# Kernel tuning notes

Hardware: AMD Instinct MI355X
Metric: run time of the kernel (lower is better)

## Reference

```python
import jax, jax.numpy as jnp
import numpy as np


def setup_inputs() -> dict:
    key = jax.random.key(0)
    k1, k2, k3, k4 = jax.random.split(key, 4)
    B, T, D, U = 32, 2048, 256, 256
    x = jax.random.normal(k1, (B, T, D), dtype=jnp.float32)
    Wz = jax.random.normal(k2, (D + U, U), dtype=jnp.float32) * 0.05
    Wr = jax.random.normal(k3, (D + U, U), dtype=jnp.float32) * 0.05
    Wh = jax.random.normal(k4, (D + U, U), dtype=jnp.float32) * 0.05
    return {"x": x, "Wz": Wz, "Wr": Wr, "Wh": Wh}


def reference(x, Wz, Wr, Wh):
    # GRU recurrence: z = sigmoid([x,h] Wz); r = sigmoid([x,h] Wr);
    # h_hat = tanh([x, r*h] Wh); h' = z*h + (1-z)*h_hat
    B = x.shape[0]
    U = Wz.shape[1]
    h0 = jnp.zeros((B, U), dtype=x.dtype)

    def step(h, x_t):
        x_h = jnp.concatenate([x_t, h], axis=-1)          # [B, D+U]
        z = jax.nn.sigmoid(x_h @ Wz)                       # [B, U]
        r = jax.nn.sigmoid(x_h @ Wr)                       # [B, U]
        x_rh = jnp.concatenate([x_t, r * h], axis=-1)      # [B, D+U]
        h_hat = jnp.tanh(x_rh @ Wh)                        # [B, U]
        new_h = z * h + (1.0 - z) * h_hat
        return new_h, new_h

    xs = jnp.swapaxes(x, 0, 1)                             # [T, B, D]
    _, ys = jax.lax.scan(step, h0, xs)                     # ys: [T, B, U]
    return jnp.swapaxes(ys, 0, 1)                          # [B, T, U]
```

## Files before the change

kernel.cpp:

```cpp
#include <hip/hip_runtime.h>
#include <hip/hip_fp16.h>
#include <stdint.h>

#define NB 32
#define NT 2048
#define ND 256
#define NU 256

typedef _Float16 f16x2 __attribute__((ext_vector_type(2)));

__device__ __forceinline__ float fdot2u(uint32_t a, uint32_t b, float c) {
#if __has_builtin(__builtin_amdgcn_fdot2)
  return __builtin_amdgcn_fdot2(__builtin_bit_cast(f16x2, a),
                                __builtin_bit_cast(f16x2, b), c, false);
#else
  f16x2 av = __builtin_bit_cast(f16x2, a);
  f16x2 bv = __builtin_bit_cast(f16x2, b);
  return c + (float)av.x * (float)bv.x + (float)av.y * (float)bv.y;
#endif
}

__device__ __forceinline__ uint32_t packh2(float lo, float hi) {
  f16x2 p;
  p.x = (_Float16)lo;
  p.y = (_Float16)hi;
  return __builtin_bit_cast(uint32_t, p);
}

__device__ __forceinline__ uint4 ldg_opaque(const uint4* p) {
  uint4 r;
  asm volatile("global_load_dwordx4 %0, %1, off" : "=v"(r) : "v"(p));
  return r;
}

__device__ __forceinline__ float rcp_fast(float x) { return __builtin_amdgcn_rcpf(x); }
__device__ __forceinline__ float sigmoid_fast(float x) {
  return rcp_fast(1.f + __expf(-x));
}
__device__ __forceinline__ float tanh_fast(float x) {
  return 1.f - 2.f * rcp_fast(1.f + __expf(2.f * x));
}

struct SRec {
  float hbuf[NU];
  alignas(16) uint32_t h2[NU / 2];
  alignas(16) uint32_t rh2[NU / 2];
  float psh[NU];
};
struct SGemm {
  float a[64][132];
  float b[64][68];
};

__global__ __launch_bounds__(512, 2)
__attribute__((amdgpu_waves_per_eu(2, 2)))
void gru_combined(
    const float* __restrict__ x, const float* __restrict__ Wz,
    const float* __restrict__ Wr, const float* __restrict__ Wh,
    const uint32_t* __restrict__ Wf16, float* __restrict__ hstate,
    float* __restrict__ out, const float* __restrict__ Gsrc,
    float* __restrict__ Gdst, int t0r, int t0g, int recCnt, int chunkT) {
  __shared__ union SM {
    SRec r;
    SGemm g;
  } sm;
  const int tid = threadIdx.x;

  if ((int)blockIdx.x < recCnt) {
    const int b = blockIdx.x;
    const int u = tid & (NU - 1);
    const int role = tid >> 8;

    uint4 wfull[32], wh[16];
    const uint4* W4 = (const uint4*)Wf16;
    const uint4* pf = W4 + (size_t)role * (NU * 32) + u * 32;
#pragma unroll
    for (int j = 0; j < 32; j++) wfull[j] = ldg_opaque(pf + j);
    const uint4* ph = W4 + (size_t)2 * (NU * 32) + u * 32 + role * 16;
#pragma unroll
    for (int j = 0; j < 16; j++) wh[j] = ldg_opaque(ph + j);

    float hu = hstate[b * NU + u];
    if (tid < NU) sm.r.hbuf[tid] = hu;
    __syncthreads();
    if (tid < NU / 2) sm.r.h2[tid] = packh2(sm.r.hbuf[2 * tid], sm.r.hbuf[2 * tid + 1]);
    __syncthreads();

    asm volatile("s_waitcnt vmcnt(0)" ::: "memory");
    __builtin_amdgcn_sched_barrier(0);

    const float* Gb = Gsrc + (size_t)b * NU + u;
    float* outp = out + ((size_t)b * NT + t0r) * NU + u;
    float hprev = hu;

    for (int tt = 0; tt < chunkT; ++tt) {
      float g0, g1 = 0.f;
      {
        const float* Gt = Gb + (size_t)(tt * 3) * NB * NU;
        if (role == 0) {
          g0 = Gt[0];
          g1 = Gt[2 * NB * NU];
        } else {
          g0 = Gt[NB * NU];
        }
      }
      float a0 = 0.f, a1 = 0.f, a2 = 0.f, a3 = 0.f;
#pragma unroll
      for (int jb = 0; jb < 32; jb++) {
        uint4 hv = *(const uint4*)&sm.r.h2[jb * 4];
        a0 = fdot2u(wfull[jb].x, hv.x, a0);
        a1 = fdot2u(wfull[jb].y, hv.y, a1);
        a2 = fdot2u(wfull[jb].z, hv.z, a2);
        a3 = fdot2u(wfull[jb].w, hv.w, a3);
      }
      const float ssum = ((a0 + a1) + (a2 + a3)) + g0;
      float zval = 0.f;
      if (role == 1) {
        const float rr = sigmoid_fast(ssum);
        const float rh = rr * hprev;
        const float rh1 = __shfl_down(rh, 1);
        if ((u & 1) == 0) sm.r.rh2[u >> 1] = packh2(rh, rh1);
      } else {
        zval = sigmoid_fast(ssum);
      }
      __syncthreads();
      float c0 = 0.f, c1 = 0.f, c2 = 0.f, c3 = 0.f;
#pragma unroll
      for (int jb = 0; jb < 16; jb++) {
        uint4 rv = *(const uint4*)&sm.r.rh2[(role * 16 + jb) * 4];
        c0 = fdot2u(wh[jb].x, rv.x, c0);
        c1 = fdot2u(wh[jb].y, rv.y, c1);
        c2 = fdot2u(wh[jb].z, rv.z, c2);
        c3 = fdot2u(wh[jb].w, rv.w, c3);
      }
      const float csum = (c0 + c1) + (c2 + c3);
      if (role == 1) sm.r.psh[u] = csum;
      __syncthreads();
      if (role == 0) {
        const float hh = tanh_fast(g1 + csum + sm.r.psh[u]);
        const float hn = zval * hprev + (1.f - zval) * hh;
        hprev = hn;
        outp[0] = hn;
        sm.r.hbuf[u] = hn;
        const float hn1 = __shfl_down(hn, 1);
        if ((u & 1) == 0) sm.r.h2[u >> 1] = packh2(hn, hn1);
      }
      outp += NU;
      __syncthreads();
      if (role == 1) hprev = sm.r.hbuf[u];
    }
    if (role == 0) hstate[b * NU + u] = hprev;

  } else if (Gdst != nullptr) {
    const int gg = (int)blockIdx.x - recCnt;
    const int mtile = gg / 12;
    const int ntile = gg - mtile * 12;
    const int g = ntile >> 2;
    const int u0 = (ntile & 3) * 64;
    const float* Wg = (g == 0) ? Wz : ((g == 1) ? Wr : Wh);
    const int ty = tid >> 4;
    const int tx = tid & 15;
    const int mbase = mtile * 128;
    float acc[4][4] = {{0.f}};

    for (int kk = 0; kk < 4; ++kk) {
      const int k0 = kk * 64;
      __syncthreads();
      {
        const int ml = tid & 127;
        const int kq = tid >> 7;
        const int m = mbase + ml;
        const int bb = m / chunkT;
        const int tt = m - bb * chunkT;
        const float* xp = x + ((size_t)bb * NT + t0g + tt) * ND + k0 + kq * 16;
#pragma unroll
        for (int v = 0; v < 4; ++v) {
          float4 xv = ((const float4*)xp)[v];
          sm.g.a[kq * 16 + v * 4 + 0][ml] = xv.x;
          sm.g.a[kq * 16 + v * 4 + 1][ml] = xv.y;
          sm.g.a[kq * 16 + v * 4 + 2][ml] = xv.z;
          sm.g.a[kq * 16 + v * 4 + 3][ml] = xv.w;
        }
      }
      {
        const int nl = (tid & 15) * 4;
        const int kr = tid >> 4;
#pragma unroll
        for (int s = 0; s < 2; ++s) {
          const int krow = kr + s * 32;
          float4 wv = *(const float4*)&Wg[(size_t)(k0 + krow) * NU + u0 + nl];
          *(float4*)&sm.g.b[krow][nl] = wv;
        }
      }
      __syncthreads();
#pragma unroll 8
      for (int k = 0; k < 64; ++k) {
        const float4 av = *(const float4*)&sm.g.a[k][ty * 4];
        const float4 bv = *(const float4*)&sm.g.b[k][tx * 4];
        acc[0][0] += av.x * bv.x; acc[0][1] += av.x * bv.y; acc[0][2] += av.x * bv.z; acc[0][3] += av.x * bv.w;
        acc[1][0] += av.y * bv.x; acc[1][1] += av.y * bv.y; acc[1][2] += av.y * bv.z; acc[1][3] += av.y * bv.w;
        acc[2][0] += av.z * bv.x; acc[2][1] += av.z * bv.y; acc[2][2] += av.z * bv.z; acc[2][3] += av.z * bv.w;
        acc[3][0] += av.w * bv.x; acc[3][1] += av.w * bv.y; acc[3][2] += av.w * bv.z; acc[3][3] += av.w * bv.w;
      }
    }
#pragma unroll
    for (int i = 0; i < 4; ++i) {
      const int m = mbase + ty * 4 + i;
      const int bb = m / chunkT;
      const int tt = m - bb * chunkT;
      float4 val;
      val.x = acc[i][0]; val.y = acc[i][1]; val.z = acc[i][2]; val.w = acc[i][3];
      *(float4*)&Gdst[((size_t)(tt * 3 + g) * NB + bb) * NU + u0 + tx * 4] = val;
    }
  }
}

__global__ void gru_prep(const float* __restrict__ Wz, const float* __restrict__ Wr,
                         const float* __restrict__ Wh, uint32_t* __restrict__ Wf16,
                         float* __restrict__ hstate) {
  const int idx = blockIdx.x * 256 + threadIdx.x;
  const int NW = 3 * NU * 128;
  if (idx < NW) {
    const int g = idx / (NU * 128);
    const int rem = idx - g * (NU * 128);
    const int u = rem >> 7;
    const int p = rem & 127;
    const float* Wg = (g == 0) ? Wz : ((g == 1) ? Wr : Wh);
    float w0 = Wg[(size_t)(ND + 2 * p) * NU + u];
    float w1 = Wg[(size_t)(ND + 2 * p + 1) * NU + u];
    Wf16[idx] = packh2(w0, w1);
  } else {
    const int j = idx - NW;
    if (j < NB * NU) hstate[j] = 0.f;
  }
}

extern "C" void kernel_launch(void* const* d_in, const int* in_sizes, int n_in,
                              void* d_out, int out_size, void* d_ws, size_t ws_size,
                              hipStream_t stream) {
  (void)in_sizes; (void)n_in; (void)out_size;
  const float* x = (const float*)d_in[0];
  const float* Wz = (const float*)d_in[1];
  const float* Wr = (const float*)d_in[2];
  const float* Wh = (const float*)d_in[3];
  float* out = (float*)d_out;

  int ct = 8;
  const int cands[6] = {256, 128, 64, 32, 16, 8};
  for (int i = 0; i < 6; ++i) {
    size_t need = 2ull * cands[i] * 3 * NB * NU * 4 + (1u << 20);
    if (need <= ws_size) { ct = cands[i]; break; }
  }
  const int nch = NT / ct;
  const size_t chunkBytes = (size_t)ct * 3 * NB * NU * 4;

  char* wsb = (char*)d_ws;
  float* G0 = (float*)wsb;
  float* G1 = (float*)(wsb + chunkBytes);
  uint32_t* Wf16 = (uint32_t*)(wsb + 2 * chunkBytes);
  float* hstate = (float*)(wsb + 2 * chunkBytes + (size_t)3 * NU * 128 * 4);

  const int prepThreads = 3 * NU * 128 + NB * NU;
  gru_prep<<<(prepThreads + 255) / 256, 256, 0, stream>>>(Wz, Wr, Wh, Wf16, hstate);

  gru_combined<<<3 * ct, 512, 0, stream>>>(x, Wz, Wr, Wh, Wf16, hstate, out,
                                           nullptr, G0, 0, 0, 0, ct);
  for (int k = 0; k < nch; ++k) {
    float* Gsrc = (k & 1) ? G1 : G0;
    float* Gdst = (k & 1) ? G0 : G1;
    const int gemmOn = (k + 1 < nch) ? 1 : 0;
    gru_combined<<<32 + (gemmOn ? 3 * ct : 0), 512, 0, stream>>>(
        x, Wz, Wr, Wh, Wf16, hstate, out, Gsrc, gemmOn ? Gdst : nullptr,
        k * ct, (k + 1) * ct, 32, ct);
  }
}
```

Measured before the change: 2.926 ms.

## Move candidate-gate weights to LDS and re-stream z/r weights each step

The fp16 recurrent Wh weights now live in a 128KB dynamic LDS buffer instead of per-thread registers. The z/r weights use a new packed layout and are re-issued as global loads every timestep, after the gate dot products, so they refill while the Wh phase runs. Per-step G loads become inline asm with explicit waitcnts. This frees registers at the cost of heavy per-step L2 traffic. It also forces one large-LDS block per CU, which limits occupancy for the co-scheduled GEMM blocks.

```diff
diff --git a/kernel.cpp b/kernel.cpp
--- a/kernel.cpp
+++ b/kernel.cpp
@@ -27,12 +27,6 @@
   return __builtin_bit_cast(uint32_t, p);
 }
 
-__device__ __forceinline__ uint4 ldg_opaque(const uint4* p) {
-  uint4 r;
-  asm volatile("global_load_dwordx4 %0, %1, off" : "=v"(r) : "v"(p));
-  return r;
-}
-
 __device__ __forceinline__ float rcp_fast(float x) { return __builtin_amdgcn_rcpf(x); }
 __device__ __forceinline__ float sigmoid_fast(float x) {
   return rcp_fast(1.f + __expf(-x));
@@ -41,117 +35,158 @@
   return 1.f - 2.f * rcp_fast(1.f + __expf(2.f * x));
 }
 
-struct SRec {
-  float hbuf[NU];
-  alignas(16) uint32_t h2[NU / 2];
-  alignas(16) uint32_t rh2[NU / 2];
-  float psh[NU];
-};
+#define LDS_WH 0
+#define LDS_H2 131072
+#define LDS_RH2 131584
+#define LDS_PSH 132096
+#define LDS_HBUF 133120
+#define LDS_TOTAL 134144
+
+extern __shared__ char smdyn[];
+
 struct SGemm {
   float a[64][132];
   float b[64][68];
 };
 
-__global__ __launch_bounds__(512, 2)
+#define WDECL \
+  uint4 w0, w1, w2, w3, w4, w5, w6, w7, w8, w9, w10, w11, w12, w13, w14, w15, \
+      w16, w17, w18, w19, w20, w21, w22, w23, w24, w25, w26, w27, w28, w29,   \
+      w30, w31;
+
+#define WL(i, P, OFF) \
+  asm volatile("global_load_dwordx4 %0, %1, off" OFF : "=v"(w##i) : "v"(P));
+
+#define WGRP(i0, i1, i2, i3, P) \
+  WL(i0, P, "") WL(i1, P, " offset:16") WL(i2, P, " offset:32") WL(i3, P, " offset:48")
+
+#define WISSUE \
+  WGRP(0, 1, 2, 3, pA) WGRP(4, 5, 6, 7, pB) WGRP(8, 9, 10, 11, pC) \
+  WGRP(12, 13, 14, 15, pD) WGRP(16, 17, 18, 19, pE) WGRP(20, 21, 22, 23, pF) \
+  WGRP(24, 25, 26, 27, pG) WGRP(28, 29, 30, 31, pH)
+
+#define DOTA(i)                                     \
+  {                                                 \
+    const uint4 hv = *(const uint4*)&h2L[(i) * 4];  \
+    a0 = fdot2u(w##i.x, hv.x, a0);                  \
+    a1 = fdot2u(w##i.y, hv.y, a1);                  \
+    a2 = fdot2u(w##i.z, hv.z, a2);                  \
+    a3 = fdot2u(w##i.w, hv.w, a3);                  \
+  }
+#define DOTA8(i0, i1, i2, i3, i4, i5, i6, i7) \
+  DOTA(i0) DOTA(i1) DOTA(i2) DOTA(i3) DOTA(i4) DOTA(i5) DOTA(i6) DOTA(i7)
+
+__global__ __launch_bounds__(512)
 __attribute__((amdgpu_waves_per_eu(2, 2)))
 void gru_combined(
     const float* __restrict__ x, const float* __restrict__ Wz,
     const float* __restrict__ Wr, const float* __restrict__ Wh,
-    const uint32_t* __restrict__ Wf16, float* __restrict__ hstate,
+    const uint32_t* __restrict__ Wp, float* __restrict__ hstate,
     float* __restrict__ out, const float* __restrict__ Gsrc,
     float* __restrict__ Gdst, int t0r, int t0g, int recCnt, int chunkT) {
-  __shared__ union SM {
-    SRec r;
-    SGemm g;
-  } sm;
   const int tid = threadIdx.x;
 
   if ((int)blockIdx.x < recCnt) {
     const int b = blockIdx.x;
-    const int u = tid & (NU - 1);
+    const int u = tid & 255;
     const int role = tid >> 8;
 
-    uint4 wfull[32], wh[16];
-    const uint4* W4 = (const uint4*)Wf16;
-    const uint4* pf = W4 + (size_t)role * (NU * 32) + u * 32;
-#pragma unroll
-    for (int j = 0; j < 32; j++) wfull[j] = ldg_opaque(pf + j);
-    const uint4* ph = W4 + (size_t)2 * (NU * 32) + u * 32 + role * 16;
-#pragma unroll
-    for (int j = 0; j < 16; j++) wh[j] = ldg_opaque(ph + j);
-
-    float hu = hstate[b * NU + u];
-    if (tid < NU) sm.r.hbuf[tid] = hu;
+    uint32_t* WhL = (uint32_t*)(smdyn + LDS_WH);
+    uint32_t* h2L = (uint32_t*)(smdyn + LDS_H2);
+    uint32_t* rh2L = (uint32_t*)(smdyn + LDS_RH2);
+    float* pshL = (float*)(smdyn + LDS_PSH);
+    float* hbufL = (float*)(smdyn + LDS_HBUF);
+
+    const uint4* colb = ((const uint4*)Wp) + (size_t)role * 8192 + (u << 2);
+    const uint4* pA = colb;
+    const uint4* pB = colb + 1024;
+    const uint4* pC = colb + 2048;
+    const uint4* pD = colb + 3072;
+    const uint4* pE = colb + 4096;
+    const uint4* pF = colb + 5120;
+    const uint4* pG = colb + 6144;
+    const uint4* pH = colb + 7168;
+    WDECL
+    WISSUE
+
+    {
+      const uint4* WpH4 = ((const uint4*)Wp) + 16384;
+      uint4* WhL4 = (uint4*)(smdyn + LDS_WH);
+#pragma unroll
+      for (int i = 0; i < 16; ++i) WhL4[tid + i * 512] = WpH4[tid + i * 512];
+    }
+    float hprev = hstate[b * NU + u];
+    if (tid < NU) hbufL[tid] = hprev;
     __syncthreads();
-    if (tid < NU / 2) sm.r.h2[tid] = packh2(sm.r.hbuf[2 * tid], sm.r.hbuf[2 * tid + 1]);
+    if (tid < 128) h2L[tid] = packh2(hbufL[2 * tid], hbufL[2 * tid + 1]);
     __syncthreads();
 
-    asm volatile("s_waitcnt vmcnt(0)" ::: "memory");
-    __builtin_amdgcn_sched_barrier(0);
-
-    const float* Gb = Gsrc + (size_t)b * NU + u;
+    const char* gp = (const char*)(Gsrc + (size_t)b * NU + u) +
+                     (role == 0 ? 0 : (size_t)NB * NU * 4);
+    const size_t gstride = (size_t)3 * NB * NU * 4;
     float* outp = out + ((size_t)b * NT + t0r) * NU + u;
-    float hprev = hu;
 
     for (int tt = 0; tt < chunkT; ++tt) {
-      float g0, g1 = 0.f;
-      {
-        const float* Gt = Gb + (size_t)(tt * 3) * NB * NU;
-        if (role == 0) {
-          g0 = Gt[0];
-          g1 = Gt[2 * NB * NU];
-        } else {
-          g0 = Gt[NB * NU];
-        }
-      }
+      asm volatile("s_waitcnt vmcnt(0)" ::: "memory");
+      __builtin_amdgcn_sched_barrier(0);
+      float gA, gB = 0.f;
+      asm volatile("global_load_dword %0, %1, off" : "=v"(gA) : "v"(gp));
+      if (role == 0)
+        asm volatile("global_load_dword %0, %1, off"
+                     : "=v"(gB)
+                     : "v"(gp + 2 * (size_t)NB * NU * 4));
       float a0 = 0.f, a1 = 0.f, a2 = 0.f, a3 = 0.f;
-#pragma unroll
-      for (int jb = 0; jb < 32; jb++) {
-        uint4 hv = *(const uint4*)&sm.r.h2[jb * 4];
-        a0 = fdot2u(wfull[jb].x, hv.x, a0);
-        a1 = fdot2u(wfull[jb].y, hv.y, a1);
-        a2 = fdot2u(wfull[jb].z, hv.z, a2);
-        a3 = fdot2u(wfull[jb].w, hv.w, a3);
-      }
-      const float ssum = ((a0 + a1) + (a2 + a3)) + g0;
+      DOTA8(0, 1, 2, 3, 4, 5, 6, 7)
+      DOTA8(8, 9, 10, 11, 12, 13, 14, 15)
+      DOTA8(16, 17, 18, 19, 20, 21, 22, 23)
+      DOTA8(24, 25, 26, 27, 28, 29, 30, 31)
+      asm volatile("s_waitcnt vmcnt(0)" ::: "memory");
+      __builtin_amdgcn_sched_barrier(0);
+      const float ssum = ((a0 + a1) + (a2 + a3)) + gA;
       float zval = 0.f;
-      if (role == 1) {
+      if (role == 0) {
+        zval = sigmoid_fast(ssum);
+      } else {
         const float rr = sigmoid_fast(ssum);
         const float rh = rr * hprev;
         const float rh1 = __shfl_down(rh, 1);
-        if ((u & 1) == 0) sm.r.rh2[u >> 1] = packh2(rh, rh1);
-      } else {
-        zval = sigmoid_fast(ssum);
-      }
+        if ((u & 1) == 0) rh2L[u >> 1] = packh2(rh, rh1);
+      }
+      __builtin_amdgcn_sched_barrier(0);
+      WISSUE
       __syncthreads();
       float c0 = 0.f, c1 = 0.f, c2 = 0.f, c3 = 0.f;
 #pragma unroll
-      for (int jb = 0; jb < 16; jb++) {
-        uint4 rv = *(const uint4*)&sm.r.rh2[(role * 16 + jb) * 4];
-        c0 = fdot2u(wh[jb].x, rv.x, c0);
-        c1 = fdot2u(wh[jb].y, rv.y, c1);
-        c2 = fdot2u(wh[jb].z, rv.z, c2);
-        c3 = fdot2u(wh[jb].w, rv.w, c3);
-      }
-      const float csum = (c0 + c1) + (c2 + c3);
-      if (role == 1) sm.r.psh[u] = csum;
+      for (int j = 0; j < 64; j += 4) {
+        const int k2 = (role << 6) + j;
+        const uint4 r4 = *(const uint4*)&rh2L[k2];
+        c0 = fdot2u(WhL[(k2 + 0) * 256 + u], r4.x, c0);
+        c1 = fdot2u(WhL[(k2 + 1) * 256 + u], r4.y, c1);
+        c2 = fdot2u(WhL[(k2 + 2) * 256 + u], r4.z, c2);
+        c3 = fdot2u(WhL[(k2 + 3) * 256 + u], r4.w, c3);
+      }
+      const float cown = (c0 + c1) + (c2 + c3);
+      if (role == 1) pshL[u] = cown;
       __syncthreads();
       if (role == 0) {
-        const float hh = tanh_fast(g1 + csum + sm.r.psh[u]);
+        const float hh = tanh_fast(gB + cown + pshL[u]);
         const float hn = zval * hprev + (1.f - zval) * hh;
         hprev = hn;
-        outp[0] = hn;
-        sm.r.hbuf[u] = hn;
+        asm volatile("global_store_dword %0, %1, off" ::"v"(outp), "v"(hn));
+        hbufL[u] = hn;
         const float hn1 = __shfl_down(hn, 1);
-        if ((u & 1) == 0) sm.r.h2[u >> 1] = packh2(hn, hn1);
+        if ((u & 1) == 0) h2L[u >> 1] = packh2(hn, hn1);
       }
       outp += NU;
-      __syncthreads();
-      if (role == 1) hprev = sm.r.hbuf[u];
+      gp += gstride;
+      __syncthreads();
+      if (role == 1) hprev = hbufL[u];
     }
     if (role == 0) hstate[b * NU + u] = hprev;
+    asm volatile("s_waitcnt vmcnt(0)" ::: "memory");
 
   } else if (Gdst != nullptr) {
+    SGemm& smg = *(SGemm*)smdyn;
     const int gg = (int)blockIdx.x - recCnt;
     const int mtile = gg / 12;
     const int ntile = gg - mtile * 12;
@@ -171,32 +206,32 @@
         const int kq = tid >> 7;
         const int m = mbase + ml;
         const int bb = m / chunkT;
-        const int tt = m - bb * chunkT;
-        const float* xp = x + ((size_t)bb * NT + t0g + tt) * ND + k0 + kq * 16;
+        const int ttm = m - bb * chunkT;
+        const float* xp = x + ((size_t)bb * NT + t0g + ttm) * ND + k0 + kq * 16;
 #pragma unroll
         for (int v = 0; v < 4; ++v) {
           float4 xv = ((const float4*)xp)[v];
-          sm.g.a[kq * 16 + v * 4 + 0][ml] = xv.x;
-          sm.g.a[kq * 16 + v * 4 + 1][ml] = xv.y;
-          sm.g.a[kq * 16 + v * 4 + 2][ml] = xv.z;
-          sm.g.a[kq * 16 + v * 4 + 3][ml] = xv.w;
+          smg.a[kq * 16 + v * 4 + 0][ml] = xv.x;
+          smg.a[kq * 16 + v * 4 + 1][ml] = xv.y;
+          smg.a[kq * 16 + v * 4 + 2][ml] = xv.z;
+          smg.a[kq * 16 + v * 4 + 3][ml] = xv.w;
         }
       }
       {
         const int nl = (tid & 15) * 4;
         const int kr = tid >> 4;
 #pragma unroll
-        for (int s = 0; s < 2; ++s) {
-          const int krow = kr + s * 32;
-          float4 wv = *(const float4*)&Wg[(size_t)(k0 + krow) * NU + u0 + nl];
-          *(float4*)&sm.g.b[krow][nl] = wv;
+        for (int s2 = 0; s2 < 2; ++s2) {
+          const int krow = kr + s2 * 32;
+          float4 wvv = *(const float4*)&Wg[(size_t)(k0 + krow) * NU + u0 + nl];
+          *(float4*)&smg.b[krow][nl] = wvv;
         }
       }
       __syncthreads();
 #pragma unroll 8
       for (int k = 0; k < 64; ++k) {
-        const float4 av = *(const float4*)&sm.g.a[k][ty * 4];
-        const float4 bv = *(const float4*)&sm.g.b[k][tx * 4];
+        const float4 av = *(const float4*)&smg.a[k][ty * 4];
+        const float4 bv = *(const float4*)&smg.b[k][tx * 4];
         acc[0][0] += av.x * bv.x; acc[0][1] += av.x * bv.y; acc[0][2] += av.x * bv.z; acc[0][3] += av.x * bv.w;
         acc[1][0] += av.y * bv.x; acc[1][1] += av.y * bv.y; acc[1][2] += av.y * bv.z; acc[1][3] += av.y * bv.w;
         acc[2][0] += av.z * bv.x; acc[2][1] += av.z * bv.y; acc[2][2] += av.z * bv.z; acc[2][3] += av.z * bv.w;
@@ -207,31 +242,35 @@
     for (int i = 0; i < 4; ++i) {
       const int m = mbase + ty * 4 + i;
       const int bb = m / chunkT;
-      const int tt = m - bb * chunkT;
+      const int ttm = m - bb * chunkT;
       float4 val;
       val.x = acc[i][0]; val.y = acc[i][1]; val.z = acc[i][2]; val.w = acc[i][3];
-      *(float4*)&Gdst[((size_t)(tt * 3 + g) * NB + bb) * NU + u0 + tx * 4] = val;
+      *(float4*)&Gdst[((size_t)(ttm * 3 + g) * NB + bb) * NU + u0 + tx * 4] = val;
     }
   }
 }
 
 __global__ void gru_prep(const float* __restrict__ Wz, const float* __restrict__ Wr,
-                         const float* __restrict__ Wh, uint32_t* __restrict__ Wf16,
+                         const float* __restrict__ Wh, uint32_t* __restrict__ Wp,
                          float* __restrict__ hstate) {
   const int idx = blockIdx.x * 256 + threadIdx.x;
-  const int NW = 3 * NU * 128;
-  if (idx < NW) {
-    const int g = idx / (NU * 128);
-    const int rem = idx - g * (NU * 128);
-    const int u = rem >> 7;
-    const int p = rem & 127;
-    const float* Wg = (g == 0) ? Wz : ((g == 1) ? Wr : Wh);
-    float w0 = Wg[(size_t)(ND + 2 * p) * NU + u];
-    float w1 = Wg[(size_t)(ND + 2 * p + 1) * NU + u];
-    Wf16[idx] = packh2(w0, w1);
-  } else {
-    const int j = idx - NW;
-    if (j < NB * NU) hstate[j] = 0.f;
+  if (idx < 65536) {
+    const int p = idx & 3;
+    const int c = (idx >> 2) & 3;
+    const int u = (idx >> 4) & 255;
+    const int j4 = (idx >> 12) & 7;
+    const int g = (idx >> 15) & 1;
+    const float* Wg = (g == 0) ? Wz : Wr;
+    const int k0 = (j4 * 4 + c) * 8 + 2 * p;
+    Wp[idx] = packh2(Wg[(size_t)(ND + k0) * NU + u], Wg[(size_t)(ND + k0 + 1) * NU + u]);
+  } else if (idx < 98304) {
+    const int r = idx - 65536;
+    const int u = r & 255;
+    const int k2 = r >> 8;
+    Wp[idx] = packh2(Wh[(size_t)(ND + 2 * k2) * NU + u],
+                     Wh[(size_t)(ND + 2 * k2 + 1) * NU + u]);
+  } else if (idx - 98304 < NB * NU) {
+    hstate[idx - 98304] = 0.f;
   }
 }
 
@@ -245,6 +284,9 @@
   const float* Wh = (const float*)d_in[3];
   float* out = (float*)d_out;
 
+  hipFuncSetAttribute((const void*)gru_combined,
+                      hipFuncAttributeMaxDynamicSharedMemorySize, LDS_TOTAL);
+
   int ct = 8;
   const int cands[6] = {256, 128, 64, 32, 16, 8};
   for (int i = 0; i < 6; ++i) {
@@ -257,20 +299,19 @@
   char* wsb = (char*)d_ws;
   float* G0 = (float*)wsb;
   float* G1 = (float*)(wsb + chunkBytes);
-  uint32_t* Wf16 = (uint32_t*)(wsb + 2 * chunkBytes);
-  float* hstate = (float*)(wsb + 2 * chunkBytes + (size_t)3 * NU * 128 * 4);
-
-  const int prepThreads = 3 * NU * 128 + NB * NU;
-  gru_prep<<<(prepThreads + 255) / 256, 256, 0, stream>>>(Wz, Wr, Wh, Wf16, hstate);
-
-  gru_combined<<<3 * ct, 512, 0, stream>>>(x, Wz, Wr, Wh, Wf16, hstate, out,
-                                           nullptr, G0, 0, 0, 0, ct);
+  uint32_t* Wp = (uint32_t*)(wsb + 2 * chunkBytes);
+  float* hstate = (float*)(wsb + 2 * chunkBytes + 98304ull * 4);
+
+  gru_prep<<<416, 256, 0, stream>>>(Wz, Wr, Wh, Wp, hstate);
+
+  gru_combined<<<3 * ct, 512, LDS_TOTAL, stream>>>(
+      x, Wz, Wr, Wh, Wp, hstate, out, nullptr, G0, 0, 0, 0, ct);
   for (int k = 0; k < nch; ++k) {
     float* Gsrc = (k & 1) ? G1 : G0;
     float* Gdst = (k & 1) ? G0 : G1;
     const int gemmOn = (k + 1 < nch) ? 1 : 0;
-    gru_combined<<<32 + (gemmOn ? 3 * ct : 0), 512, 0, stream>>>(
-        x, Wz, Wr, Wh, Wf16, hstate, out, Gsrc, gemmOn ? Gdst : nullptr,
+    gru_combined<<<32 + (gemmOn ? 3 * ct : 0), 512, LDS_TOTAL, stream>>>(
+        x, Wz, Wr, Wh, Wp, hstate, out, Gsrc, gemmOn ? Gdst : nullptr,
         k * ct, (k + 1) * ct, 32, ct);
   }
 }
```

Result: slower. 9.758 ms (+233.5%).
